# Kernel optimization log

Hardware: AMD Instinct MI355X
Metric: run time of the kernel (lower is better)

The kernel has to match this reference:

```python
import math
import jax, jax.numpy as jnp
import numpy as np

# ---- static config ----
B, S, HID = 2, 8192, 1024
H, D = 8, 128                      # num_heads, head_dim = hidden // heads
CHUNK = 128                        # attention_chunk_size
PAST = 128 - 1                     # attention_context_left - 1
FUT = 128                          # attention_context_right
CTX = CHUNK + PAST + FUT           # 383
POS = CTX + 1                      # relative position table length (rel_shift pads to CTX+1)
CAP = 50.0                         # attention_logit_cap
Q_SCALE = D ** (-0.5) / math.log(2.0)
K_SCALE = math.log1p(math.e) / math.log(2.0)
NB = S // CHUNK                    # 64 blocks (S divisible by chunk -> no tail padding)


def setup_inputs() -> dict:
    key = jax.random.key(0)
    ks = jax.random.split(key, 8)
    s = 0.02
    return {
        "hidden_states": jax.random.normal(ks[0], (B, S, HID), jnp.float32),
        "position_embeddings": jax.random.normal(ks[1], (POS, HID), jnp.float32),
        "Wq": jax.random.normal(ks[2], (HID, H * D), jnp.float32) * s,
        "Wk": jax.random.normal(ks[3], (HID, H * D), jnp.float32) * s,
        "Wv": jax.random.normal(ks[4], (HID, H * D), jnp.float32) * s,
        "Wrel": jax.random.normal(ks[5], (HID, H * D), jnp.float32) * s,
        "Wpost": jax.random.normal(ks[6], (HID, HID), jnp.float32) * s,
        "per_dim_scale": jax.random.normal(ks[7], (D,), jnp.float32) * 0.1,
    }


def reference(hidden_states, position_embeddings, Wq, Wk, Wv, Wrel, Wpost, per_dim_scale):
    # projections (clipped-linear clamps are +/-inf -> no-ops); bias-free linears
    q = (hidden_states @ Wq).reshape(B, S, H, D)
    k = (hidden_states @ Wk).reshape(B, S, H, D)
    v = (hidden_states @ Wv).reshape(B, S, H, D)

    q = q * (Q_SCALE * jax.nn.softplus(per_dim_scale))  # per-dim scaling fused into q
    k = k * K_SCALE

    # _convert_to_block: [B, NB, CHUNK, H, D] (S % CHUNK == 0 -> no pad)
    qb = q.reshape(B, NB, CHUNK, H, D)

    # _extract_block_context: pad (PAST, FUT + CHUNK - 1) then unfold window=CTX step=CHUNK
    pad = ((0, 0), (PAST, FUT + CHUNK - 1), (0, 0), (0, 0))
    kp = jnp.pad(k, pad)
    vp = jnp.pad(v, pad)
    idx = jnp.arange(NB)[:, None] * CHUNK + jnp.arange(CTX)[None, :]  # [NB, CTX]
    kc = kp[:, idx]  # [B, NB, CTX, H, D]
    vc = vp[:, idx]  # [B, NB, CTX, H, D]

    # relative keys: [POS, H, D]
    rel_k = (position_embeddings @ Wrel).reshape(POS, H, D)

    # content scores: [B, H, NB, CHUNK, CTX]
    ac = jnp.einsum('bnchd,bnkhd->bhnck', qb, kc)
    # position scores before shift: [B, H, NB, CHUNK, POS]
    bd = jnp.einsum('bnchd,phd->bhncp', qb, rel_k)
    # Transformer-XL rel_shift (POS == CTX+1 so pad amount is zero)
    bd = bd.reshape(B, H, NB, CHUNK * POS)[..., : CHUNK * CTX]
    bd = bd.reshape(B, H, NB, CHUNK, CTX)

    # tanh soft-cap + softmax (no attention_mask)
    logits = jnp.tanh((ac + bd) / CAP) * CAP
    attn = jax.nn.softmax(logits, axis=-1)

    # weighted values -> [B, NB, CHUNK, H, D] -> [B, S, HID]
    out = jnp.einsum('bhnck,bnkhd->bnchd', attn, vc).reshape(B, S, H * D)
    return out @ Wpost
```

## Files before the change

kernel.cpp:

```cpp
#include <hip/hip_runtime.h>
#include <cmath>


using bf16x8 = __attribute__((ext_vector_type(8))) short;
using f32x4  = __attribute__((ext_vector_type(4))) float;
using s16x4  = __attribute__((ext_vector_type(4))) short;

__device__ __forceinline__ short f2bf(float f) {
  unsigned u = __float_as_uint(f);
  u = (u + 0x7FFF + ((u >> 16) & 1)) >> 16;
  return (short)u;
}
__device__ __forceinline__ float bf2f(unsigned short s) {
  return __uint_as_float(((unsigned)s) << 16);
}

__device__ __forceinline__ void gl16(void* lds, const void* gptr) {
  __builtin_amdgcn_global_load_lds(
      (const __attribute__((address_space(1))) unsigned int*)gptr,
      (__attribute__((address_space(3))) unsigned int*)lds, 16, 0, 0);
}

__global__ void cvt_bf16_k(const float* __restrict__ in, short* __restrict__ out, int n) {
  int i = (blockIdx.x * 256 + threadIdx.x) * 4;
  if (i + 3 < n) {
    float4 v = *(const float4*)&in[i];
    s16x4 o;
    o[0] = f2bf(v.x); o[1] = f2bf(v.y); o[2] = f2bf(v.z); o[3] = f2bf(v.w);
    *(s16x4*)&out[i] = o;
  }
}

__global__ void wtrans_k(const float* __restrict__ W, short* __restrict__ Wt) {
  __shared__ float T[64 * 65];
  const int tid = threadIdx.x;
  const int bx = blockIdx.x, by = blockIdx.y;
#pragma unroll
  for (int it = 0; it < 4; ++it) {
    int ci = it * 256 + tid;
    int k = ci >> 4, n4 = (ci & 15) * 4;
    float4 v = *(const float4*)&W[(size_t)(by * 64 + k) * 1024 + bx * 64 + n4];
    T[k * 65 + n4 + 0] = v.x;
    T[k * 65 + n4 + 1] = v.y;
    T[k * 65 + n4 + 2] = v.z;
    T[k * 65 + n4 + 3] = v.w;
  }
  __syncthreads();
#pragma unroll
  for (int it = 0; it < 2; ++it) {
    int co = it * 256 + tid;
    int nn = co >> 3, k8 = (co & 7) * 8;
    bf16x8 o;
#pragma unroll
    for (int jj = 0; jj < 8; ++jj) o[jj] = f2bf(T[(k8 + jj) * 65 + nn]);
    *(bf16x8*)&Wt[(size_t)(bx * 64 + nn) * 1024 + by * 64 + k8] = o;
  }
}

__global__ void qscale_k(const float* __restrict__ pds, float* __restrict__ qs, double qsb) {
  int d = threadIdx.x;
  double x = (double)pds[d];
  qs[d] = (float)(qsb * log1p(exp(x)));
}

__global__ void vpadzero_k(short* __restrict__ vpadT) {
  int row = blockIdx.x;
  int t = threadIdx.x;
  int key = (t < 127) ? t : (8192 + t);
  vpadT[(size_t)row * 8448 + key] = 0;
}

__global__ __launch_bounds__(256, 3)
void qkv_fused_k(const short* __restrict__ A, const short* __restrict__ Bt3,
                 short* __restrict__ q_bf, short* __restrict__ kpad,
                 short* __restrict__ vpadT,
                 const float* __restrict__ qsc, float kscale) {
  __shared__ __align__(16) short As[128 * 32];
  __shared__ __align__(16) short Bs[128 * 32];
  __shared__ __align__(16) short Tv[128 * 136];

  const int tid = threadIdx.x;
  const int lane = tid & 63, wid = tid >> 6;
  const int q4 = lane >> 4, l16 = lane & 15;
  const int wr = wid >> 1, wc = wid & 1;

  const int id = blockIdx.x;
  const int xcd = id & 7, local = id >> 3;
  const int mm = local / 24, nn = local - mm * 24;
  const int m0 = (xcd * 16 + mm) * 128;
  const int w = nn >> 3, nc = nn & 7;
  const short* Bt = Bt3 + ((size_t)w * 1024 + nc * 128) * 1024;

  const f32x4 z4 = {0.f, 0.f, 0.f, 0.f};
  f32x4 acc[4][4];
#pragma unroll
  for (int i = 0; i < 4; ++i)
#pragma unroll
    for (int j = 0; j < 4; ++j) acc[i][j] = z4;

  const int r0 = tid >> 2, s0_ = (tid & 3) * 8;

  for (int kk = 0; kk < 1024; kk += 32) {
    __syncthreads();
    gl16(&As[tid * 8],         A  + (size_t)(m0 + r0) * 1024 + kk + s0_);
    gl16(&Bs[tid * 8],         Bt + (size_t)r0 * 1024 + kk + s0_);
    gl16(&As[(256 + tid) * 8], A  + (size_t)(m0 + 64 + r0) * 1024 + kk + s0_);
    gl16(&Bs[(256 + tid) * 8], Bt + (size_t)(64 + r0) * 1024 + kk + s0_);
    __syncthreads();
    bf16x8 af[4], bfv[4];
#pragma unroll
    for (int i = 0; i < 4; ++i)
      af[i] = *(const bf16x8*)&As[(wr * 64 + i * 16 + l16) * 32 + q4 * 8];
#pragma unroll
    for (int j = 0; j < 4; ++j)
      bfv[j] = *(const bf16x8*)&Bs[(wc * 64 + j * 16 + l16) * 32 + q4 * 8];
#pragma unroll
    for (int i = 0; i < 4; ++i)
#pragma unroll
      for (int j = 0; j < 4; ++j)
        acc[i][j] = __builtin_amdgcn_mfma_f32_16x16x32_bf16(af[i], bfv[j], acc[i][j], 0, 0, 0);
  }

  float qsv[4];
  if (w == 0) {
#pragma unroll
    for (int j = 0; j < 4; ++j) qsv[j] = qsc[wc * 64 + j * 16 + l16];
  }

#pragma unroll
  for (int i = 0; i < 4; ++i) {
#pragma unroll
    for (int j = 0; j < 4; ++j) {
#pragma unroll
      for (int rg = 0; rg < 4; ++rg) {
        const int row = m0 + wr * 64 + i * 16 + q4 * 4 + rg;
        const int d = wc * 64 + j * 16 + l16;
        const int h = nc;
        const float v = acc[i][j][rg];
        if (w == 0) {
          int b = row >> 13, s = row & 8191;
          int n = s >> 7, c = s & 127;
          q_bf[((size_t)(((b * 64 + n) * 8 + h) * 128 + c)) * 128 + d] = f2bf(v * qsv[j]);
        } else if (w == 1) {
          int b = row >> 13, s = row & 8191;
          kpad[((size_t)(b * 8 + h) * 8448 + 127 + s) * 128 + d] = f2bf(v * kscale);
        } else {
          int sl = wr * 64 + i * 16 + q4 * 4 + rg;
          Tv[d * 136 + sl] = f2bf(v);
        }
      }
    }
  }

  if (w == 2) {
    __syncthreads();
    const int b = m0 >> 13, ss = m0 & 8191, h = nc;
#pragma unroll
    for (int it = 0; it < 8; ++it) {
      int co = it * 256 + tid;
      int d = co >> 4, s8 = (co & 15) * 8;
      *(bf16x8*)&vpadT[((size_t)(b * 8 + h) * 128 + d) * 8448 + 127 + ss + s8] =
          *(const bf16x8*)&Tv[d * 136 + s8];
    }
  }
}

__global__ __launch_bounds__(256, 3)
void post_gemm_k(const short* __restrict__ A, const short* __restrict__ Bt,
                 float* __restrict__ outf) {
  __shared__ __align__(16) short As[128 * 32];
  __shared__ __align__(16) short Bs[128 * 32];

  const int tid = threadIdx.x;
  const int lane = tid & 63, wid = tid >> 6;
  const int q4 = lane >> 4, l16 = lane & 15;
  const int wr = wid >> 1, wc = wid & 1;

  const int id = blockIdx.x;
  const int xcd = id & 7, local = id >> 3;
  const int mm = local >> 3, nn = local & 7;
  const int m0 = (xcd * 16 + mm) * 128, n0 = nn * 128;

  const f32x4 z4 = {0.f, 0.f, 0.f, 0.f};
  f32x4 acc[4][4];
#pragma unroll
  for (int i = 0; i < 4; ++i)
#pragma unroll
    for (int j = 0; j < 4; ++j) acc[i][j] = z4;

  const int r0 = tid >> 2, s0_ = (tid & 3) * 8;

  for (int kk = 0; kk < 1024; kk += 32) {
    __syncthreads();
    gl16(&As[tid * 8],         A  + (size_t)(m0 + r0) * 1024 + kk + s0_);
    gl16(&Bs[tid * 8],         Bt + (size_t)(n0 + r0) * 1024 + kk + s0_);
    gl16(&As[(256 + tid) * 8], A  + (size_t)(m0 + 64 + r0) * 1024 + kk + s0_);
    gl16(&Bs[(256 + tid) * 8], Bt + (size_t)(n0 + 64 + r0) * 1024 + kk + s0_);
    __syncthreads();
    bf16x8 af[4], bfv[4];
#pragma unroll
    for (int i = 0; i < 4; ++i)
      af[i] = *(const bf16x8*)&As[(wr * 64 + i * 16 + l16) * 32 + q4 * 8];
#pragma unroll
    for (int j = 0; j < 4; ++j)
      bfv[j] = *(const bf16x8*)&Bs[(wc * 64 + j * 16 + l16) * 32 + q4 * 8];
#pragma unroll
    for (int i = 0; i < 4; ++i)
#pragma unroll
      for (int j = 0; j < 4; ++j)
        acc[i][j] = __builtin_amdgcn_mfma_f32_16x16x32_bf16(af[i], bfv[j], acc[i][j], 0, 0, 0);
  }

#pragma unroll
  for (int i = 0; i < 4; ++i)
#pragma unroll
    for (int j = 0; j < 4; ++j)
#pragma unroll
      for (int rg = 0; rg < 4; ++rg) {
        const int row = m0 + wr * 64 + i * 16 + q4 * 4 + rg;
        const int col = n0 + wc * 64 + j * 16 + l16;
        outf[(size_t)row * 1024 + col] = acc[i][j][rg];
      }
}

__global__ __launch_bounds__(256, 2)
void rel_gemm_k(const short* __restrict__ A, const short* __restrict__ Bt,
                short* __restrict__ relk) {
  __shared__ __align__(16) short As[128 * 32];
  __shared__ __align__(16) short Bs[128 * 32];

  const int tid = threadIdx.x;
  const int lane = tid & 63, wid = tid >> 6;
  const int q4 = lane >> 4, l16 = lane & 15;
  const int wr = wid >> 1, wc = wid & 1;
  const int m0 = blockIdx.x * 128, n0 = blockIdx.y * 128;

  const f32x4 z4 = {0.f, 0.f, 0.f, 0.f};
  f32x4 acc[4][4];
#pragma unroll
  for (int i = 0; i < 4; ++i)
#pragma unroll
    for (int j = 0; j < 4; ++j) acc[i][j] = z4;

  const int r0 = tid >> 2, s0_ = (tid & 3) * 8;
  for (int kk = 0; kk < 1024; kk += 32) {
    __syncthreads();
    gl16(&As[tid * 8],         A  + (size_t)(m0 + r0) * 1024 + kk + s0_);
    gl16(&Bs[tid * 8],         Bt + (size_t)(n0 + r0) * 1024 + kk + s0_);
    gl16(&As[(256 + tid) * 8], A  + (size_t)(m0 + 64 + r0) * 1024 + kk + s0_);
    gl16(&Bs[(256 + tid) * 8], Bt + (size_t)(n0 + 64 + r0) * 1024 + kk + s0_);
    __syncthreads();
    bf16x8 af[4], bfv[4];
#pragma unroll
    for (int i = 0; i < 4; ++i)
      af[i] = *(const bf16x8*)&As[(wr * 64 + i * 16 + l16) * 32 + q4 * 8];
#pragma unroll
    for (int j = 0; j < 4; ++j)
      bfv[j] = *(const bf16x8*)&Bs[(wc * 64 + j * 16 + l16) * 32 + q4 * 8];
#pragma unroll
    for (int i = 0; i < 4; ++i)
#pragma unroll
      for (int j = 0; j < 4; ++j)
        acc[i][j] = __builtin_amdgcn_mfma_f32_16x16x32_bf16(af[i], bfv[j], acc[i][j], 0, 0, 0);
  }

#pragma unroll
  for (int i = 0; i < 4; ++i)
#pragma unroll
    for (int j = 0; j < 4; ++j)
#pragma unroll
      for (int rg = 0; rg < 4; ++rg) {
        const int row = m0 + wr * 64 + i * 16 + q4 * 4 + rg;
        const int col = n0 + wc * 64 + j * 16 + l16;
        int h = col >> 7, d = col & 127;
        relk[(size_t)(h * 384 + row) * 128 + d] = f2bf(acc[i][j][rg]);
      }
}

__global__ __launch_bounds__(256, 2)
void bd_gemm_k(const short* __restrict__ qb_b, const short* __restrict__ relk,
               short* __restrict__ bds) {
  __shared__ __align__(16) short As[128 * 32];
  __shared__ __align__(16) short Bs[128 * 32];
  const int tid = threadIdx.x;
  const int lane = tid & 63, wid = tid >> 6;
  const int q4 = lane >> 4, l16 = lane & 15;
  const int wr = wid >> 1, wc = wid & 1;
  const int p0 = blockIdx.x * 128;
  const int nh = blockIdx.y;
  const int h = nh & 7;
  const short* A = qb_b + (size_t)nh * 16384;
  const short* Bt = relk + (size_t)h * (384 * 128);
  short* bdo = bds + (size_t)nh * 49152;

  const f32x4 z4 = {0.f, 0.f, 0.f, 0.f};
  f32x4 acc[4][4];
#pragma unroll
  for (int i = 0; i < 4; ++i)
#pragma unroll
    for (int j = 0; j < 4; ++j) acc[i][j] = z4;

  const int r0 = tid >> 2, s0_ = (tid & 3) * 8;
  for (int kk = 0; kk < 128; kk += 32) {
    __syncthreads();
    gl16(&As[tid * 8],         A  + (size_t)r0 * 128 + kk + s0_);
    gl16(&Bs[tid * 8],         Bt + (size_t)(p0 + r0) * 128 + kk + s0_);
    gl16(&As[(256 + tid) * 8], A  + (size_t)(64 + r0) * 128 + kk + s0_);
    gl16(&Bs[(256 + tid) * 8], Bt + (size_t)(p0 + 64 + r0) * 128 + kk + s0_);
    __syncthreads();
    bf16x8 af[4], bfv[4];
#pragma unroll
    for (int i = 0; i < 4; ++i)
      af[i] = *(const bf16x8*)&As[(wr * 64 + i * 16 + l16) * 32 + q4 * 8];
#pragma unroll
    for (int j = 0; j < 4; ++j)
      bfv[j] = *(const bf16x8*)&Bs[(wc * 64 + j * 16 + l16) * 32 + q4 * 8];
#pragma unroll
    for (int i = 0; i < 4; ++i)
#pragma unroll
      for (int j = 0; j < 4; ++j)
        acc[i][j] = __builtin_amdgcn_mfma_f32_16x16x32_bf16(af[i], bfv[j], acc[i][j], 0, 0, 0);
  }

#pragma unroll
  for (int i = 0; i < 4; ++i)
#pragma unroll
    for (int j = 0; j < 4; ++j)
#pragma unroll
      for (int rg = 0; rg < 4; ++rg) {
        int r = wr * 64 + i * 16 + q4 * 4 + rg;
        int p = p0 + wc * 64 + j * 16 + l16;
        int t = r + p;
        int c = (t < 383) ? r : (r + 1);
        int k = (t < 383) ? t : (t - 383);
        if (c < 128) {
          int tt = k >> 7, jj = (k >> 4) & 7, ll = k & 15;
          int wa = c >> 5, ia = (c >> 4) & 1, qa = (c >> 2) & 3, ra = c & 3;
          bdo[((((size_t)tt * 8 + jj) * 256) + wa * 64 + qa * 16 + ll) * 8 + ia * 4 + ra] =
              f2bf(acc[i][j][rg]);
        }
      }
}

__global__ __launch_bounds__(256, 2)
void attn_k(const short* __restrict__ qb_b, const short* __restrict__ kpad,
            const short* __restrict__ vpadT, const short* __restrict__ bds,
            short* __restrict__ attnout, int b) {
  __shared__ __align__(16) short Ks[4 * 128 * 32];
  __shared__ __align__(16) short Ps[128 * 136];

  const int tid = threadIdx.x;
  const int lane = tid & 63, wid = tid >> 6;
  const int q4 = lane >> 4, l16 = lane & 15;
  const int bx = blockIdx.x;
  const int n = bx >> 3, h = bx & 7;

  const short* qtile = qb_b + (size_t)bx * 16384;
  const short* kbase = kpad + ((size_t)(b * 8 + h) * 8448 + n * 128) * 128;
  const short* vtb = vpadT + (size_t)(b * 8 + h) * 128 * 8448 + n * 128;
  const short* bdb = bds + (size_t)bx * 49152;

#pragma unroll
  for (int it = 0; it < 8; ++it) {
    int ci = it * 256 + tid;
    int dc = ci >> 9, rr = (ci >> 2) & 127, sub = (ci & 3) * 8;
    gl16(&Ks[ci * 8], qtile + rr * 128 + dc * 32 + sub);
  }
  __syncthreads();
  bf16x8 qf[2][4];
#pragma unroll
  for (int i = 0; i < 2; ++i)
#pragma unroll
    for (int dc = 0; dc < 4; ++dc)
      qf[i][dc] = *(const bf16x8*)&Ks[dc * 4096 + (wid * 32 + i * 16 + l16) * 32 + q4 * 8];

  const f32x4 z4 = {0.f, 0.f, 0.f, 0.f};
  f32x4 acco[2][8];
#pragma unroll
  for (int i = 0; i < 2; ++i)
#pragma unroll
    for (int j = 0; j < 8; ++j) acco[i][j] = z4;
  float rsum[2][4] = {};

  for (int t = 0; t < 3; ++t) {
    __syncthreads();
#pragma unroll
    for (int it = 0; it < 8; ++it) {
      int ci = it * 256 + tid;
      int dc = ci >> 9, rr = (ci >> 2) & 127, sub = (ci & 3) * 8;
      gl16(&Ks[ci * 8], kbase + (size_t)(t * 128 + rr) * 128 + dc * 32 + sub);
    }

    bf16x8 bdv[8];
#pragma unroll
    for (int j = 0; j < 8; ++j)
      bdv[j] = *(const bf16x8*)&bdb[(((size_t)t * 8 + j) * 256 + wid * 64 + lane) * 8];

    __syncthreads();

    f32x4 accs[2][8];
#pragma unroll
    for (int i = 0; i < 2; ++i)
#pragma unroll
      for (int j = 0; j < 8; ++j) accs[i][j] = z4;
#pragma unroll
    for (int dc = 0; dc < 4; ++dc) {
      bf16x8 kf[8];
#pragma unroll
      for (int j = 0; j < 8; ++j)
        kf[j] = *(const bf16x8*)&Ks[dc * 4096 + (j * 16 + l16) * 32 + q4 * 8];
#pragma unroll
      for (int i = 0; i < 2; ++i)
#pragma unroll
        for (int j = 0; j < 8; ++j)
          accs[i][j] = __builtin_amdgcn_mfma_f32_16x16x32_bf16(qf[i][dc], kf[j], accs[i][j], 0, 0, 0);
    }

#pragma unroll
    for (int i = 0; i < 2; ++i) {
#pragma unroll
      for (int j = 0; j < 8; ++j) {
        const int kg = t * 128 + j * 16 + l16;
#pragma unroll
        for (int rg = 0; rg < 4; ++rg) {
          float sv = accs[i][j][rg] + bf2f((unsigned short)bdv[j][i * 4 + rg]);
          float tt = exp2f(sv * 0.057707801635558534f);
          float wgt = exp2f(-144.26950408889634f * __fdividef(1.0f, tt + 1.0f));
          wgt = (kg < 383) ? wgt : 0.0f;
          accs[i][j][rg] = wgt;
          rsum[i][rg] += wgt;
        }
      }
    }
    __syncthreads();

#pragma unroll
    for (int it = 0; it < 8; ++it) {
      int ci = it * 256 + tid;
      int kc = ci >> 9, dd = (ci >> 2) & 127, sub = (ci & 3) * 8;
      gl16(&Ks[ci * 8], vtb + (size_t)dd * 8448 + t * 128 + kc * 32 + sub);
    }
#pragma unroll
    for (int i = 0; i < 2; ++i)
#pragma unroll
      for (int j = 0; j < 8; ++j)
#pragma unroll
        for (int rg = 0; rg < 4; ++rg) {
          int c = wid * 32 + i * 16 + q4 * 4 + rg;
          int kl = j * 16 + l16;
          Ps[c * 136 + kl] = f2bf(accs[i][j][rg]);
        }
    __syncthreads();

#pragma unroll
    for (int kc = 0; kc < 4; ++kc) {
      bf16x8 pf[2], vf[8];
#pragma unroll
      for (int i = 0; i < 2; ++i)
        pf[i] = *(const bf16x8*)&Ps[(wid * 32 + i * 16 + l16) * 136 + kc * 32 + q4 * 8];
#pragma unroll
      for (int j = 0; j < 8; ++j)
        vf[j] = *(const bf16x8*)&Ks[kc * 4096 + (j * 16 + l16) * 32 + q4 * 8];
#pragma unroll
      for (int i = 0; i < 2; ++i)
#pragma unroll
        for (int j = 0; j < 8; ++j)
          acco[i][j] = __builtin_amdgcn_mfma_f32_16x16x32_bf16(pf[i], vf[j], acco[i][j], 0, 0, 0);
    }
  }

  float rinv[2][4];
#pragma unroll
  for (int i = 0; i < 2; ++i)
#pragma unroll
    for (int rg = 0; rg < 4; ++rg) {
      float rs = rsum[i][rg];
      rs += __shfl_xor(rs, 1);
      rs += __shfl_xor(rs, 2);
      rs += __shfl_xor(rs, 4);
      rs += __shfl_xor(rs, 8);
      rinv[i][rg] = __fdividef(1.0f, rs);
    }
#pragma unroll
  for (int i = 0; i < 2; ++i)
#pragma unroll
    for (int j = 0; j < 8; ++j)
#pragma unroll
      for (int rg = 0; rg < 4; ++rg) {
        int srow = n * 128 + wid * 32 + i * 16 + q4 * 4 + rg;
        int col = h * 128 + j * 16 + l16;
        attnout[((size_t)b * 8192 + srow) * 1024 + col] = f2bf(acco[i][j][rg] * rinv[i][rg]);
      }
}

extern "C" void kernel_launch(void* const* d_in, const int* in_sizes, int n_in,
                              void* d_out, int out_size, void* d_ws, size_t ws_size,
                              hipStream_t stream) {
  (void)in_sizes; (void)n_in; (void)out_size; (void)ws_size;
  const float* hs    = (const float*)d_in[0];
  const float* pemb  = (const float*)d_in[1];
  const float* Wq    = (const float*)d_in[2];
  const float* Wk    = (const float*)d_in[3];
  const float* Wv    = (const float*)d_in[4];
  const float* Wrel  = (const float*)d_in[5];
  const float* Wpost = (const float*)d_in[6];
  const float* pds   = (const float*)d_in[7];
  float* out = (float*)d_out;

  char* w = (char*)d_ws;
  auto alloc = [&](size_t bytes) -> char* {
    char* p = w; w += (bytes + 255) & ~(size_t)255; return p;
  };
  short* hs_bf   = (short*)alloc((size_t)16384 * 1024 * 2);
  short* pos_bf  = (short*)alloc((size_t)384 * 1024 * 2);
  short* Wq_t    = (short*)alloc((size_t)1024 * 1024 * 2);
  short* Wk_t    = (short*)alloc((size_t)1024 * 1024 * 2);
  short* Wv_t    = (short*)alloc((size_t)1024 * 1024 * 2);
  short* Wrel_t  = (short*)alloc((size_t)1024 * 1024 * 2);
  short* Wpost_t = (short*)alloc((size_t)1024 * 1024 * 2);
  float* qsc     = (float*)alloc(512);
  short* q_bf    = (short*)alloc((size_t)2 * 64 * 8 * 128 * 128 * 2);
  short* kpad    = (short*)alloc((size_t)2 * 8 * 8448 * 128 * 2);
  short* vpadT   = (short*)alloc((size_t)2 * 8 * 128 * 8448 * 2);
  short* relk    = (short*)alloc((size_t)8 * 384 * 128 * 2);
  short* bds     = (short*)alloc((size_t)64 * 8 * 128 * 384 * 2);
  short* attnout = hs_bf;

  const float kscale = (float)(log1p(exp(1.0)) / log(2.0));
  const double qsb = (1.0 / sqrt(128.0)) / log(2.0);

  cvt_bf16_k<<<16384, 256, 0, stream>>>(hs, hs_bf, 16384 * 1024);
  cvt_bf16_k<<<384, 256, 0, stream>>>(pemb, pos_bf, 384 * 1024);
  dim3 tg(16, 16);
  wtrans_k<<<tg, 256, 0, stream>>>(Wq, Wq_t);
  wtrans_k<<<tg, 256, 0, stream>>>(Wk, Wk_t);
  wtrans_k<<<tg, 256, 0, stream>>>(Wv, Wv_t);
  wtrans_k<<<tg, 256, 0, stream>>>(Wrel, Wrel_t);
  wtrans_k<<<tg, 256, 0, stream>>>(Wpost, Wpost_t);
  qscale_k<<<1, 128, 0, stream>>>(pds, qsc, qsb);
  hipMemsetAsync(kpad, 0, (size_t)2 * 8 * 8448 * 128 * 2, stream);
  vpadzero_k<<<2048, 256, 0, stream>>>(vpadT);

  qkv_fused_k<<<3072, 256, 0, stream>>>(hs_bf, Wq_t, q_bf, kpad, vpadT, qsc, kscale);
  rel_gemm_k<<<dim3(3, 8), 256, 0, stream>>>(pos_bf, Wrel_t, relk);

  for (int b = 0; b < 2; ++b) {
    const short* qb_b = q_bf + (size_t)b * 64 * 8 * 128 * 128;
    bd_gemm_k<<<dim3(3, 512), 256, 0, stream>>>(qb_b, relk, bds);
    attn_k<<<512, 256, 0, stream>>>(qb_b, kpad, vpadT, bds, attnout, b);
  }

  post_gemm_k<<<1024, 256, 0, stream>>>(attnout, Wpost_t, out);
}
```

Measured before the change: 557.3 us.

## Split attention query tile into two 64-row halves per block

The attention kernel now handles 64 query rows per block instead of 128, doubling the grid to 1024 blocks per batch and raising launch bounds to 3 blocks per CU. Each wave owns 16 query rows, so per-thread accumulators and the P staging buffer shrink, which should allow more resident blocks and better latency hiding. In exchange, each K and V context tile is loaded once per half-tile, doubling K/V global and LDS traffic.

```diff
diff --git a/kernel.cpp b/kernel.cpp
--- a/kernel.cpp
+++ b/kernel.cpp
@@ -342,45 +342,42 @@
       }
 }
 
-__global__ __launch_bounds__(256, 2)
+__global__ __launch_bounds__(256, 3)
 void attn_k(const short* __restrict__ qb_b, const short* __restrict__ kpad,
             const short* __restrict__ vpadT, const short* __restrict__ bds,
             short* __restrict__ attnout, int b) {
   __shared__ __align__(16) short Ks[4 * 128 * 32];
-  __shared__ __align__(16) short Ps[128 * 136];
+  __shared__ __align__(16) short Ps[64 * 136];
 
   const int tid = threadIdx.x;
   const int lane = tid & 63, wid = tid >> 6;
   const int q4 = lane >> 4, l16 = lane & 15;
   const int bx = blockIdx.x;
-  const int n = bx >> 3, h = bx & 7;
-
-  const short* qtile = qb_b + (size_t)bx * 16384;
+  const int qh = bx & 1, nh = bx >> 1;
+  const int n = nh >> 3, h = nh & 7;
+
+  const short* qtile = qb_b + (size_t)nh * 16384 + qh * 64 * 128;
   const short* kbase = kpad + ((size_t)(b * 8 + h) * 8448 + n * 128) * 128;
   const short* vtb = vpadT + (size_t)(b * 8 + h) * 128 * 8448 + n * 128;
-  const short* bdb = bds + (size_t)bx * 49152;
-
-#pragma unroll
-  for (int it = 0; it < 8; ++it) {
+  const short* bdb = bds + (size_t)nh * 49152;
+
+#pragma unroll
+  for (int it = 0; it < 4; ++it) {
     int ci = it * 256 + tid;
-    int dc = ci >> 9, rr = (ci >> 2) & 127, sub = (ci & 3) * 8;
+    int dc = ci >> 8, rr = (ci >> 2) & 63, sub = (ci & 3) * 8;
     gl16(&Ks[ci * 8], qtile + rr * 128 + dc * 32 + sub);
   }
   __syncthreads();
-  bf16x8 qf[2][4];
-#pragma unroll
-  for (int i = 0; i < 2; ++i)
-#pragma unroll
-    for (int dc = 0; dc < 4; ++dc)
-      qf[i][dc] = *(const bf16x8*)&Ks[dc * 4096 + (wid * 32 + i * 16 + l16) * 32 + q4 * 8];
+  bf16x8 qf[4];
+#pragma unroll
+  for (int dc = 0; dc < 4; ++dc)
+    qf[dc] = *(const bf16x8*)&Ks[dc * 2048 + (wid * 16 + l16) * 32 + q4 * 8];
 
   const f32x4 z4 = {0.f, 0.f, 0.f, 0.f};
-  f32x4 acco[2][8];
-#pragma unroll
-  for (int i = 0; i < 2; ++i)
-#pragma unroll
-    for (int j = 0; j < 8; ++j) acco[i][j] = z4;
-  float rsum[2][4] = {};
+  f32x4 acco[8];
+#pragma unroll
+  for (int j = 0; j < 8; ++j) acco[j] = z4;
+  float rsum[4] = {};
 
   for (int t = 0; t < 3; ++t) {
     __syncthreads();
@@ -391,18 +388,17 @@
       gl16(&Ks[ci * 8], kbase + (size_t)(t * 128 + rr) * 128 + dc * 32 + sub);
     }
 
-    bf16x8 bdv[8];
+    s16x4 bdv[8];
 #pragma unroll
     for (int j = 0; j < 8; ++j)
-      bdv[j] = *(const bf16x8*)&bdb[(((size_t)t * 8 + j) * 256 + wid * 64 + lane) * 8];
-
-    __syncthreads();
-
-    f32x4 accs[2][8];
-#pragma unroll
-    for (int i = 0; i < 2; ++i)
-#pragma unroll
-      for (int j = 0; j < 8; ++j) accs[i][j] = z4;
+      bdv[j] = *(const s16x4*)&bdb[((((size_t)t * 8 + j) * 256) +
+                 (qh * 2 + (wid >> 1)) * 64 + q4 * 16 + l16) * 8 + (wid & 1) * 4];
+
+    __syncthreads();
+
+    f32x4 accs[8];
+#pragma unroll
+    for (int j = 0; j < 8; ++j) accs[j] = z4;
 #pragma unroll
     for (int dc = 0; dc < 4; ++dc) {
       bf16x8 kf[8];
@@ -410,26 +406,21 @@
       for (int j = 0; j < 8; ++j)
         kf[j] = *(const bf16x8*)&Ks[dc * 4096 + (j * 16 + l16) * 32 + q4 * 8];
 #pragma unroll
-      for (int i = 0; i < 2; ++i)
-#pragma unroll
-        for (int j = 0; j < 8; ++j)
-          accs[i][j] = __builtin_amdgcn_mfma_f32_16x16x32_bf16(qf[i][dc], kf[j], accs[i][j], 0, 0, 0);
-    }
-
-#pragma unroll
-    for (int i = 0; i < 2; ++i) {
-#pragma unroll
-      for (int j = 0; j < 8; ++j) {
-        const int kg = t * 128 + j * 16 + l16;
-#pragma unroll
-        for (int rg = 0; rg < 4; ++rg) {
-          float sv = accs[i][j][rg] + bf2f((unsigned short)bdv[j][i * 4 + rg]);
-          float tt = exp2f(sv * 0.057707801635558534f);
-          float wgt = exp2f(-144.26950408889634f * __fdividef(1.0f, tt + 1.0f));
-          wgt = (kg < 383) ? wgt : 0.0f;
-          accs[i][j][rg] = wgt;
-          rsum[i][rg] += wgt;
-        }
+      for (int j = 0; j < 8; ++j)
+        accs[j] = __builtin_amdgcn_mfma_f32_16x16x32_bf16(qf[dc], kf[j], accs[j], 0, 0, 0);
+    }
+
+#pragma unroll
+    for (int j = 0; j < 8; ++j) {
+      const int kg = t * 128 + j * 16 + l16;
+#pragma unroll
+      for (int rg = 0; rg < 4; ++rg) {
+        float sv = accs[j][rg] + bf2f((unsigned short)bdv[j][rg]);
+        float tt = exp2f(sv * 0.057707801635558534f);
+        float wgt = exp2f(-144.26950408889634f * __fdividef(1.0f, tt + 1.0f));
+        wgt = (kg < 383) ? wgt : 0.0f;
+        accs[j][rg] = wgt;
+        rsum[rg] += wgt;
       }
     }
     __syncthreads();
@@ -441,56 +432,46 @@
       gl16(&Ks[ci * 8], vtb + (size_t)dd * 8448 + t * 128 + kc * 32 + sub);
     }
 #pragma unroll
-    for (int i = 0; i < 2; ++i)
-#pragma unroll
-      for (int j = 0; j < 8; ++j)
-#pragma unroll
-        for (int rg = 0; rg < 4; ++rg) {
-          int c = wid * 32 + i * 16 + q4 * 4 + rg;
-          int kl = j * 16 + l16;
-          Ps[c * 136 + kl] = f2bf(accs[i][j][rg]);
-        }
+    for (int j = 0; j < 8; ++j)
+#pragma unroll
+      for (int rg = 0; rg < 4; ++rg) {
+        int c = wid * 16 + q4 * 4 + rg;
+        int kl = j * 16 + l16;
+        Ps[c * 136 + kl] = f2bf(accs[j][rg]);
+      }
     __syncthreads();
 
 #pragma unroll
     for (int kc = 0; kc < 4; ++kc) {
-      bf16x8 pf[2], vf[8];
-#pragma unroll
-      for (int i = 0; i < 2; ++i)
-        pf[i] = *(const bf16x8*)&Ps[(wid * 32 + i * 16 + l16) * 136 + kc * 32 + q4 * 8];
+      bf16x8 pf, vf[8];
+      pf = *(const bf16x8*)&Ps[(wid * 16 + l16) * 136 + kc * 32 + q4 * 8];
 #pragma unroll
       for (int j = 0; j < 8; ++j)
         vf[j] = *(const bf16x8*)&Ks[kc * 4096 + (j * 16 + l16) * 32 + q4 * 8];
 #pragma unroll
-      for (int i = 0; i < 2; ++i)
-#pragma unroll
-        for (int j = 0; j < 8; ++j)
-          acco[i][j] = __builtin_amdgcn_mfma_f32_16x16x32_bf16(pf[i], vf[j], acco[i][j], 0, 0, 0);
-    }
-  }
-
-  float rinv[2][4];
-#pragma unroll
-  for (int i = 0; i < 2; ++i)
+      for (int j = 0; j < 8; ++j)
+        acco[j] = __builtin_amdgcn_mfma_f32_16x16x32_bf16(pf, vf[j], acco[j], 0, 0, 0);
+    }
+  }
+
+  float rinv[4];
+#pragma unroll
+  for (int rg = 0; rg < 4; ++rg) {
+    float rs = rsum[rg];
+    rs += __shfl_xor(rs, 1);
+    rs += __shfl_xor(rs, 2);
+    rs += __shfl_xor(rs, 4);
+    rs += __shfl_xor(rs, 8);
+    rinv[rg] = __fdividef(1.0f, rs);
+  }
+#pragma unroll
+  for (int j = 0; j < 8; ++j)
 #pragma unroll
     for (int rg = 0; rg < 4; ++rg) {
-      float rs = rsum[i][rg];
-      rs += __shfl_xor(rs, 1);
-      rs += __shfl_xor(rs, 2);
-      rs += __shfl_xor(rs, 4);
-      rs += __shfl_xor(rs, 8);
-      rinv[i][rg] = __fdividef(1.0f, rs);
-    }
-#pragma unroll
-  for (int i = 0; i < 2; ++i)
-#pragma unroll
-    for (int j = 0; j < 8; ++j)
-#pragma unroll
-      for (int rg = 0; rg < 4; ++rg) {
-        int srow = n * 128 + wid * 32 + i * 16 + q4 * 4 + rg;
-        int col = h * 128 + j * 16 + l16;
-        attnout[((size_t)b * 8192 + srow) * 1024 + col] = f2bf(acco[i][j][rg] * rinv[i][rg]);
-      }
+      int srow = n * 128 + qh * 64 + wid * 16 + q4 * 4 + rg;
+      int col = h * 128 + j * 16 + l16;
+      attnout[((size_t)b * 8192 + srow) * 1024 + col] = f2bf(acco[j][rg] * rinv[rg]);
+    }
 }
 
 extern "C" void kernel_launch(void* const* d_in, const int* in_sizes, int n_in,
@@ -547,7 +528,7 @@
   for (int b = 0; b < 2; ++b) {
     const short* qb_b = q_bf + (size_t)b * 64 * 8 * 128 * 128;
     bd_gemm_k<<<dim3(3, 512), 256, 0, stream>>>(qb_b, relk, bds);
-    attn_k<<<512, 256, 0, stream>>>(qb_b, kpad, vpadT, bds, attnout, b);
+    attn_k<<<1024, 256, 0, stream>>>(qb_b, kpad, vpadT, bds, attnout, b);
   }
 
   post_gemm_k<<<1024, 256, 0, stream>>>(attnout, Wpost_t, out);
```

New measurement: 550.2 us. No clear change (-1.3%).
